# Optimization experiments

Hardware: AMD Instinct MI355X
Metric: run time of the kernel (lower is better)

## Reference

```python
import jax, jax.numpy as jnp
import numpy as np

TOP_N = 0.15  # ResultsErasing(top_n=0.15) and MCPA self.ratio usage


def setup_inputs() -> dict:
    key = jax.random.key(0)
    k1, k2, k3 = jax.random.split(key, 3)
    N, C, H, W = 16, 9, 512, 512
    inp = jax.random.normal(k1, (N, C, H, W), dtype=jnp.float32)   # net1 logits
    x = jax.random.normal(k2, (N, 1, H, W), dtype=jnp.float32)     # raw image
    ratio = jax.random.uniform(k3, (N,), dtype=jnp.float32)        # per-sample erase ratio
    return {"inp": inp, "x": x, "ratio": ratio}


def reference(inp, x, ratio):
    """ResultsErasing: per-(sample,channel) top-k threshold, scatter-zero mask.

    torch semantics:
      f_p  = int(ratio[n] * H * W)
      k    = int(f_p * TOP_N)                  # same k for every channel of sample n
      thr  = k-th largest of inp[n, c]         (thr = 1 if k == 0)
      x2[n, :][inp[n, c] > thr] = 0  for every channel c  -> OR over channels
    """
    N, C, H, W = inp.shape
    HW = H * W
    flat = inp.reshape(N, C, HW)
    sorted_desc = -jnp.sort(-flat, axis=-1)                      # [N, C, HW] descending
    f_p = jnp.floor(ratio * HW)                                  # int(ratio[n]*H*W)
    k = jnp.floor(f_p * TOP_N).astype(jnp.int32)                 # [N]
    idx = jnp.clip(k - 1, 0, HW - 1)[:, None, None]              # [N,1,1]
    thr = jnp.take_along_axis(sorted_desc, jnp.broadcast_to(idx, (N, C, 1)), axis=-1)[..., 0]  # [N,C]
    thr = jnp.where(k[:, None] == 0, jnp.asarray(1.0, inp.dtype), thr)
    # OR over input channels: any logit channel above its threshold erases the pixel
    mask = jnp.any(flat > thr[:, :, None], axis=1).reshape(N, 1, H, W)
    return jnp.where(mask, jnp.zeros((), x.dtype), x)
```

## Files before the change

### kernel.cpp

```cpp
#include <hip/hip_runtime.h>
#include <stdint.h>

#define NS 16
#define CHN 9
#define NC 144
#define HW 262144
#define HW4 65536
#define NBINS 704u
#define HSTRIDE 708
#define PREF_LO 0xBF40u

#define NCOPY 4
#define CSTRIDE 708

#define OFF_HIST 0
#define OFF_META 1631232
#define OFF_BMP  1631664

__device__ __forceinline__ unsigned fkey(float f) {
  unsigned u = __float_as_uint(f);
  unsigned m = (unsigned)((int)u >> 31) | 0x80000000u;
  return u ^ m;
}

__global__ __launch_bounds__(256) void k_hist(const float* __restrict__ inp,
                                              unsigned* __restrict__ hist) {
  __shared__ unsigned lh[NCOPY * CSTRIDE];
  int plane = blockIdx.x >> 4;
  int sub = blockIdx.x & 15;
  for (int i = threadIdx.x; i < NCOPY * CSTRIDE; i += 256) lh[i] = 0u;
  __syncthreads();
  unsigned cbase = (threadIdx.x & (NCOPY - 1)) * CSTRIDE;
  const float4* base = (const float4*)inp + (size_t)plane * HW4 + (size_t)sub * 4096;
#pragma unroll
  for (int it = 0; it < 16; it += 8) {
    float4 v[8];
#pragma unroll
    for (int j = 0; j < 8; ++j) v[j] = base[(it + j) * 256 + threadIdx.x];
#pragma unroll
    for (int j = 0; j < 8; ++j) {
      float e[4] = {v[j].x, v[j].y, v[j].z, v[j].w};
#pragma unroll
      for (int q = 0; q < 4; ++q) {
        unsigned bin = (fkey(e[q]) >> 16) - PREF_LO;
        if (bin < 0x8000u)
          atomicAdd(&lh[cbase + (bin < NBINS ? bin : NBINS)], 1u);
      }
    }
  }
  __syncthreads();
  unsigned* gh = hist + (size_t)blockIdx.x * HSTRIDE;
  for (int i = threadIdx.x; i < HSTRIDE; i += 256)
    gh[i] = lh[i] + lh[CSTRIDE + i] + lh[2 * CSTRIDE + i] + lh[3 * CSTRIDE + i];
}

__global__ __launch_bounds__(256) void k_scan(const unsigned* __restrict__ hist,
                                              const float* __restrict__ ratio,
                                              unsigned* __restrict__ meta) {
  int ch = blockIdx.x;
  int t = threadIdx.x;
  unsigned* Dm = meta;
  unsigned* Pm = meta + NC;
  unsigned* Km = meta + 2 * NC;
  float r = ratio[ch / CHN];
  float fp = floorf(r * 262144.0f);
  int k = (int)floorf(fp * 0.15f);
  if (k <= 0) {
    if (t == 0) { Dm[ch] = 0xBF800000u;
                  Pm[ch] = 0xFFFFFFFFu; Km[ch] = 0u; }
    return;
  }
  unsigned b0 = 0, b1 = 0, b2 = 0, b3 = 0;
  if (4 * t < HSTRIDE) {
#pragma unroll
    for (int sub = 0; sub < 16; ++sub) {
      const uint4 q = *(const uint4*)(hist + (size_t)(ch * 16 + sub) * HSTRIDE + 4 * t);
      b0 += q.x; b1 += q.y; b2 += q.z; b3 += q.w;
    }
  }
  unsigned own = b0 + b1 + b2 + b3;
  int lane = t & 63;
  unsigned v = own;
#pragma unroll
  for (int off = 1; off < 64; off <<= 1) {
    unsigned o = __shfl_down(v, off, 64);
    v += (lane + off < 64) ? o : 0u;
  }
  __shared__ unsigned wt[4];
  if (lane == 0) wt[t >> 6] = v;
  __syncthreads();
  unsigned add = 0;
  for (int w2 = (t >> 6) + 1; w2 < 4; ++w2) add += wt[w2];
  unsigned incl = v + add;
  unsigned above = incl - own;
  unsigned uk = (unsigned)k;
  if (t == 0 && incl < uk) {
    Dm[ch] = 0xFFFFFFFFu; Pm[ch] = 0xFFFFFFFFu; Km[ch] = 0u;
  }
  if (incl >= uk && above < uk) {
    unsigned bins[4] = {b0, b1, b2, b3};
    unsigned cum = above;
    for (int j = 3; j >= 0; --j) {
      unsigned c = bins[j];
      if (cum + c >= uk) {
        int b = 4 * t + j;
        if (b >= (int)NBINS) {
          Dm[ch] = 0xFFFFFFFFu; Pm[ch] = 0xFFFFFFFFu; Km[ch] = 0u;
        } else {
          unsigned pref = PREF_LO + (unsigned)b;
          Dm[ch] = (pref << 16) | 0xFFFFu;
          Pm[ch] = pref;
          Km[ch] = uk - cum;
        }
        break;
      }
      cum += c;
    }
  }
}

__global__ __launch_bounds__(256) void k_mask(const float* __restrict__ inp,
                                              const float* __restrict__ x,
                                              const unsigned* __restrict__ meta,
                                              unsigned long long* __restrict__ bmp,
                                              float* __restrict__ out) {
  int b = blockIdx.x;
  int n = b >> 8;
  int p4 = ((b & 255) << 8) + threadIdx.x;
  const unsigned* Dm = meta;
  const unsigned* Pm = meta + NC;
  int lane = threadIdx.x & 63;
  size_t wbase = (size_t)(b & 255) * 4 + (threadIdx.x >> 6);

  float4 xv = ((const float4*)x)[(size_t)n * HW4 + p4];
  float4 v[CHN];
#pragma unroll
  for (int c = 0; c < CHN; ++c)
    v[c] = ((const float4*)inp)[(size_t)(n * CHN + c) * HW4 + p4];

  unsigned m0 = 0u, m1 = 0u, m2 = 0u, m3 = 0u;
#pragma unroll
  for (int c = 0; c < CHN; ++c) {
    int ch = n * CHN + c;
    unsigned D = Dm[ch], P = Pm[ch];
    unsigned k0 = fkey(v[c].x), k1 = fkey(v[c].y), k2 = fkey(v[c].z), k3 = fkey(v[c].w);
    m0 |= (k0 > D); m1 |= (k1 > D); m2 |= (k2 > D); m3 |= (k3 > D);
    bool isc = ((k0 >> 16) == P) | ((k1 >> 16) == P) |
               ((k2 >> 16) == P) | ((k3 >> 16) == P);
    unsigned long long bal = __ballot(isc);
    if (lane == 0) bmp[(size_t)ch * 1024 + wbase] = bal;
  }
  float4 ov;
  ov.x = m0 ? 0.0f : xv.x;
  ov.y = m1 ? 0.0f : xv.y;
  ov.z = m2 ? 0.0f : xv.z;
  ov.w = m3 ? 0.0f : xv.w;
  ((float4*)out)[(size_t)n * HW4 + p4] = ov;
}

__global__ __launch_bounds__(256) void k_resolve(const float* __restrict__ inp,
                                                 const unsigned* __restrict__ meta,
                                                 const unsigned long long* __restrict__ bmp,
                                                 float* __restrict__ out) {
  int ch = blockIdx.x;
  int t = threadIdx.x;
  int lane = t & 63;
  unsigned P = meta[NC + ch];
  if (P == 0xFFFFFFFFu) return;
  unsigned kp = meta[2 * NC + ch];
  int n = ch / CHN;
  __shared__ unsigned s_grp[4096];
  __shared__ unsigned s_pix[4096];
  __shared__ unsigned short s_lo[4096];
  __shared__ unsigned h[256];
  __shared__ unsigned wt[4];
  __shared__ unsigned s_ng, s_nc, s_hb, s_kpp, s_thr;
  if (t == 0) { s_ng = 0u; s_nc = 0u; }
  __syncthreads();
  const unsigned long long* w = bmp + (size_t)ch * 1024;
  for (int i = t; i < 1024; i += 256) {
    unsigned long long word = w[i];
    while (word) {
      int bit = __ffsll((long long)word) - 1;
      unsigned idx = atomicAdd(&s_ng, 1u);
      if (idx < 4096u) s_grp[idx] = (unsigned)(i * 64 + bit);
      word &= word - 1;
    }
  }
  __syncthreads();
  unsigned ng = min(s_ng, 4096u);
  for (unsigned i = t; i < ng; i += 256) {
    unsigned g = s_grp[i];
    float4 v = ((const float4*)inp)[(size_t)ch * HW4 + g];
    unsigned kk[4] = {fkey(v.x), fkey(v.y), fkey(v.z), fkey(v.w)};
#pragma unroll
    for (int j = 0; j < 4; ++j) {
      if ((kk[j] >> 16) == P) {
        unsigned idx = atomicAdd(&s_nc, 1u);
        if (idx < 4096u) {
          s_pix[idx] = g * 4 + (unsigned)j;
          s_lo[idx] = (unsigned short)(kk[j] & 0xFFFFu);
        }
      }
    }
  }
  __syncthreads();
  unsigned cnt = min(s_nc, 4096u);
  h[t] = 0u;
  __syncthreads();
  for (unsigned i = t; i < cnt; i += 256) atomicAdd(&h[s_lo[i] >> 8], 1u);
  __syncthreads();
  {
    unsigned own = h[t];
    unsigned v = own;
#pragma unroll
    for (int off = 1; off < 64; off <<= 1) {
      unsigned o = __shfl_down(v, off, 64);
      v += (lane + off < 64) ? o : 0u;
    }
    if (lane == 0) wt[t >> 6] = v;
    __syncthreads();
    unsigned add = 0;
    for (int w2 = (t >> 6) + 1; w2 < 4; ++w2) add += wt[w2];
    unsigned incl = v + add;
    unsigned above = incl - own;
    if (incl >= kp && above < kp) {
      s_hb = (unsigned)t;
      s_kpp = kp - above;
    }
  }
  __syncthreads();
  unsigned hb = s_hb, kpp = s_kpp;
  h[t] = 0u;
  __syncthreads();
  for (unsigned i = t; i < cnt; i += 256) {
    unsigned l = s_lo[i];
    if ((l >> 8) == hb) atomicAdd(&h[l & 0xFFu], 1u);
  }
  __syncthreads();
  {
    unsigned own = h[t];
    unsigned v = own;
#pragma unroll
    for (int off = 1; off < 64; off <<= 1) {
      unsigned o = __shfl_down(v, off, 64);
      v += (lane + off < 64) ? o : 0u;
    }
    if (lane == 0) wt[t >> 6] = v;
    __syncthreads();
    unsigned add = 0;
    for (int w2 = (t >> 6) + 1; w2 < 4; ++w2) add += wt[w2];
    unsigned incl = v + add;
    unsigned above = incl - own;
    if (incl >= kpp && above < kpp) s_thr = (hb << 8) | (unsigned)t;
  }
  __syncthreads();
  unsigned thr_lo = s_thr;
  for (unsigned i = t; i < cnt; i += 256) {
    if ((unsigned)s_lo[i] > thr_lo) out[(size_t)n * HW + s_pix[i]] = 0.0f;
  }
}

extern "C" void kernel_launch(void* const* d_in, const int* in_sizes, int n_in,
                              void* d_out, int out_size, void* d_ws, size_t ws_size,
                              hipStream_t stream) {
  (void)in_sizes; (void)n_in; (void)out_size; (void)ws_size;
  const float* inp = (const float*)d_in[0];
  const float* x = (const float*)d_in[1];
  const float* ratio = (const float*)d_in[2];
  float* out = (float*)d_out;
  unsigned* ws = (unsigned*)d_ws;

  unsigned* hist = ws + OFF_HIST;
  unsigned* meta = ws + OFF_META;
  unsigned long long* bmp = (unsigned long long*)(ws + OFF_BMP);

  k_hist<<<NC * 16, 256, 0, stream>>>(inp, hist);
  k_scan<<<NC, 256, 0, stream>>>(hist, ratio, meta);
  k_mask<<<NS * 256, 256, 0, stream>>>(inp, x, meta, bmp, out);
  k_resolve<<<NC, 256, 0, stream>>>(inp, meta, bmp, out);
}
```

Before: 262.0 us.

## Merge candidate bitmaps per sample and halve histogram sub-blocks

The histogram kernel now uses 8 sub-blocks per plane instead of 16, each doing twice the work. This halves the partial-histogram traffic and the scan's reduction loads. The mask kernel now ORs the candidate flag across channels and writes one bitmap per sample instead of one per channel, cutting ballots and bitmap stores ninefold. In exchange, the resolve kernel scans a larger shared group list (capacity raised, candidate capacity lowered), so it loads more float4 groups per channel. That risks overflowing the capped buffers and giving a wrong answer when candidates are dense.

```diff
diff --git a/kernel.cpp b/kernel.cpp
--- a/kernel.cpp
+++ b/kernel.cpp
@@ -9,13 +9,17 @@
 #define NBINS 704u
 #define HSTRIDE 708
 #define PREF_LO 0xBF40u
+#define SUB 8
 
 #define NCOPY 4
 #define CSTRIDE 708
 
+#define GCAP 8192u
+#define CCAP 2048u
+
 #define OFF_HIST 0
-#define OFF_META 1631232
-#define OFF_BMP  1631664
+#define OFF_META 815616
+#define OFF_BMP  816048
 
 __device__ __forceinline__ unsigned fkey(float f) {
   unsigned u = __float_as_uint(f);
@@ -26,14 +30,14 @@
 __global__ __launch_bounds__(256) void k_hist(const float* __restrict__ inp,
                                               unsigned* __restrict__ hist) {
   __shared__ unsigned lh[NCOPY * CSTRIDE];
-  int plane = blockIdx.x >> 4;
-  int sub = blockIdx.x & 15;
+  int plane = blockIdx.x >> 3;
+  int sub = blockIdx.x & (SUB - 1);
   for (int i = threadIdx.x; i < NCOPY * CSTRIDE; i += 256) lh[i] = 0u;
   __syncthreads();
   unsigned cbase = (threadIdx.x & (NCOPY - 1)) * CSTRIDE;
-  const float4* base = (const float4*)inp + (size_t)plane * HW4 + (size_t)sub * 4096;
-#pragma unroll
-  for (int it = 0; it < 16; it += 8) {
+  const float4* base = (const float4*)inp + (size_t)plane * HW4 + (size_t)sub * 8192;
+#pragma unroll
+  for (int it = 0; it < 32; it += 8) {
     float4 v[8];
 #pragma unroll
     for (int j = 0; j < 8; ++j) v[j] = base[(it + j) * 256 + threadIdx.x];
@@ -73,8 +77,8 @@
   unsigned b0 = 0, b1 = 0, b2 = 0, b3 = 0;
   if (4 * t < HSTRIDE) {
 #pragma unroll
-    for (int sub = 0; sub < 16; ++sub) {
-      const uint4 q = *(const uint4*)(hist + (size_t)(ch * 16 + sub) * HSTRIDE + 4 * t);
+    for (int s2 = 0; s2 < SUB; ++s2) {
+      const uint4 q = *(const uint4*)(hist + (size_t)(ch * SUB + s2) * HSTRIDE + 4 * t);
       b0 += q.x; b1 += q.y; b2 += q.z; b3 += q.w;
     }
   }
@@ -100,6 +104,7 @@
   if (incl >= uk && above < uk) {
     unsigned bins[4] = {b0, b1, b2, b3};
     unsigned cum = above;
+#pragma unroll
     for (int j = 3; j >= 0; --j) {
       unsigned c = bins[j];
       if (cum + c >= uk) {
@@ -139,17 +144,18 @@
     v[c] = ((const float4*)inp)[(size_t)(n * CHN + c) * HW4 + p4];
 
   unsigned m0 = 0u, m1 = 0u, m2 = 0u, m3 = 0u;
+  bool isc = false;
 #pragma unroll
   for (int c = 0; c < CHN; ++c) {
     int ch = n * CHN + c;
     unsigned D = Dm[ch], P = Pm[ch];
     unsigned k0 = fkey(v[c].x), k1 = fkey(v[c].y), k2 = fkey(v[c].z), k3 = fkey(v[c].w);
     m0 |= (k0 > D); m1 |= (k1 > D); m2 |= (k2 > D); m3 |= (k3 > D);
-    bool isc = ((k0 >> 16) == P) | ((k1 >> 16) == P) |
-               ((k2 >> 16) == P) | ((k3 >> 16) == P);
-    unsigned long long bal = __ballot(isc);
-    if (lane == 0) bmp[(size_t)ch * 1024 + wbase] = bal;
-  }
+    isc |= ((k0 >> 16) == P) | ((k1 >> 16) == P) |
+           ((k2 >> 16) == P) | ((k3 >> 16) == P);
+  }
+  unsigned long long bal = __ballot(isc);
+  if (lane == 0) bmp[(size_t)n * 1024 + wbase] = bal;
   float4 ov;
   ov.x = m0 ? 0.0f : xv.x;
   ov.y = m1 ? 0.0f : xv.y;
@@ -169,26 +175,26 @@
   if (P == 0xFFFFFFFFu) return;
   unsigned kp = meta[2 * NC + ch];
   int n = ch / CHN;
-  __shared__ unsigned s_grp[4096];
-  __shared__ unsigned s_pix[4096];
-  __shared__ unsigned short s_lo[4096];
+  __shared__ unsigned s_grp[GCAP];
+  __shared__ unsigned s_pix[CCAP];
+  __shared__ unsigned short s_lo[CCAP];
   __shared__ unsigned h[256];
   __shared__ unsigned wt[4];
   __shared__ unsigned s_ng, s_nc, s_hb, s_kpp, s_thr;
   if (t == 0) { s_ng = 0u; s_nc = 0u; }
   __syncthreads();
-  const unsigned long long* w = bmp + (size_t)ch * 1024;
+  const unsigned long long* w = bmp + (size_t)n * 1024;
   for (int i = t; i < 1024; i += 256) {
     unsigned long long word = w[i];
     while (word) {
       int bit = __ffsll((long long)word) - 1;
       unsigned idx = atomicAdd(&s_ng, 1u);
-      if (idx < 4096u) s_grp[idx] = (unsigned)(i * 64 + bit);
+      if (idx < GCAP) s_grp[idx] = (unsigned)(i * 64 + bit);
       word &= word - 1;
     }
   }
   __syncthreads();
-  unsigned ng = min(s_ng, 4096u);
+  unsigned ng = min(s_ng, GCAP);
   for (unsigned i = t; i < ng; i += 256) {
     unsigned g = s_grp[i];
     float4 v = ((const float4*)inp)[(size_t)ch * HW4 + g];
@@ -197,7 +203,7 @@
     for (int j = 0; j < 4; ++j) {
       if ((kk[j] >> 16) == P) {
         unsigned idx = atomicAdd(&s_nc, 1u);
-        if (idx < 4096u) {
+        if (idx < CCAP) {
           s_pix[idx] = g * 4 + (unsigned)j;
           s_lo[idx] = (unsigned short)(kk[j] & 0xFFFFu);
         }
@@ -205,7 +211,7 @@
     }
   }
   __syncthreads();
-  unsigned cnt = min(s_nc, 4096u);
+  unsigned cnt = min(s_nc, CCAP);
   h[t] = 0u;
   __syncthreads();
   for (unsigned i = t; i < cnt; i += 256) atomicAdd(&h[s_lo[i] >> 8], 1u);
@@ -275,7 +281,7 @@
   unsigned* meta = ws + OFF_META;
   unsigned long long* bmp = (unsigned long long*)(ws + OFF_BMP);
 
-  k_hist<<<NC * 16, 256, 0, stream>>>(inp, hist);
+  k_hist<<<NC * SUB, 256, 0, stream>>>(inp, hist);
   k_scan<<<NC, 256, 0, stream>>>(hist, ratio, meta);
   k_mask<<<NS * 256, 256, 0, stream>>>(inp, x, meta, bmp, out);
   k_resolve<<<NC, 256, 0, stream>>>(inp, meta, bmp, out);
```

Measured after the change: 275.1 us. 5.0% more time.
